# Optimization experiments

Hardware: AMD Instinct MI355X
Metric: run time of the kernel (lower is better)

## Reference

```python
import jax, jax.numpy as jnp
import numpy as np

B, T, D_MODEL = 2, 1024, 512
EXPAND = 2
D_INNER = D_MODEL * EXPAND
STATE = 16
K_CONV = 4


def setup_inputs() -> dict:
    key = jax.random.key(0)
    ks = jax.random.split(key, 10)
    sc = lambda k, shape: jax.random.normal(k, shape, jnp.float32) * 0.02
    return {
        "x": jax.random.normal(ks[0], (B, T, D_MODEL), jnp.float32),
        "ln_g": jnp.ones((D_MODEL,), jnp.float32),
        "ln_b": jnp.zeros((D_MODEL,), jnp.float32),
        "W_in": sc(ks[1], (2 * D_INNER, D_MODEL)),
        "conv_w": sc(ks[2], (D_INNER, 1, K_CONV)),
        "conv_b": jnp.zeros((D_INNER,), jnp.float32),
        "W_B": sc(ks[3], (STATE, D_INNER)),
        "W_C": sc(ks[4], (STATE, D_INNER)),
        "W_dt": sc(ks[5], (D_INNER, D_INNER)),
        "b_dt": jax.random.uniform(ks[6], (D_INNER,), jnp.float32, -4.0, -1.0),
        # log_A init: A_diag = -(n+1) from HiPPO, log(-A_diag) = log(n+1), broadcast over d_inner
        "log_A": jnp.broadcast_to(jnp.log(jnp.arange(1, STATE + 1, dtype=jnp.float32)), (D_INNER, STATE)),
        "W_out": sc(ks[7], (D_MODEL, D_INNER)),
    }


def _silu(v):
    return v * jax.nn.sigmoid(v)


def reference(x, ln_g, ln_b, W_in, conv_w, conv_b, W_B, W_C, W_dt, b_dt, log_A, W_out):
    residual = x
    # LayerNorm (biased variance, eps=1e-5)
    mu = x.mean(-1, keepdims=True)
    var = x.var(-1, keepdims=True)
    xn = (x - mu) * jax.lax.rsqrt(var + 1e-5) * ln_g + ln_b
    # input projection and gate split
    xz = xn @ W_in.T                      # (B,T,2*D_INNER)
    x_main, z = jnp.split(xz, 2, axis=-1)
    # depthwise causal conv1d (padding=3 then slice to T == left-pad 3)
    xc = jnp.transpose(x_main, (0, 2, 1))  # (B,D_INNER,T)
    xc = jax.lax.conv_general_dilated(
        xc, conv_w, window_strides=(1,), padding=[(K_CONV - 1, 0)],
        dimension_numbers=("NCH", "OIH", "NCH"), feature_group_count=D_INNER,
    ) + conv_b[None, :, None]
    x_main = _silu(jnp.transpose(xc, (0, 2, 1)))  # (B,T,D_INNER)
    # selective scan in fp32
    xf = x_main.astype(jnp.float32)
    Bt = xf @ W_B.T                        # (B,T,N)
    Ct = xf @ W_C.T                        # (B,T,N)
    dt = jax.nn.softplus(xf @ W_dt.T + b_dt)  # (B,T,D_INNER)
    A = -jnp.exp(log_A)                    # (D_INNER,N)
    dA = jnp.exp(A[None, None] * dt[..., None])              # (B,T,D_INNER,N)
    dBx = dt[..., None] * Bt[:, :, None, :] * xf[..., None]  # (B,T,D_INNER,N)

    def comb(c1, c2):
        a1, b1 = c1
        a2, b2 = c2
        return a1 * a2, a2 * b1 + b2

    _, h = jax.lax.associative_scan(comb, (dA, dBx), axis=1)  # h_t = dA_t*h_{t-1}+dBx_t
    y = (h * Ct[:, :, None, :]).sum(-1).astype(x.dtype)       # (B,T,D_INNER)
    out = (y * _silu(z)) @ W_out.T
    return residual + out
```

## Files before the change

### kernel.cpp

```cpp
#include <hip/hip_runtime.h>

#define T_SEQ 1024
#define DM 512
#define DI 1024
#define NS 16
#define NC 32
#define CL 32

typedef __attribute__((ext_vector_type(8))) short short8;
typedef __attribute__((ext_vector_type(4))) float f32x4;
typedef unsigned short u16;
typedef unsigned int u32;

__device__ inline float b2f(u16 u) {
    unsigned v = ((unsigned)u) << 16;
    return __builtin_bit_cast(float, v);
}
__device__ inline u16 f2b(float f) {
    unsigned u = __builtin_bit_cast(unsigned, f);
    u += 0x7fff + ((u >> 16) & 1);
    return (u16)(u >> 16);
}

__device__ inline void g2l16(const u16* g, const short* l) {
    __builtin_amdgcn_global_load_lds((const __attribute__((address_space(1))) u32*)g,
                                     (__attribute__((address_space(3))) u32*)l, 16, 0, 0);
}

template<int K> __device__ __forceinline__ void vmwait() {
    if constexpr (K == 0) asm volatile("s_waitcnt vmcnt(0)" ::: "memory");
    else if constexpr (K == 2) asm volatile("s_waitcnt vmcnt(2)" ::: "memory");
}

__global__ __launch_bounds__(256) void prep_k(const float* __restrict__ Win, const float* __restrict__ Wdt,
                       const float* __restrict__ Wout, const float* __restrict__ Wb,
                       const float* __restrict__ Wc,
                       u16* __restrict__ oWin, u16* __restrict__ wCat, u16* __restrict__ oWout,
                       const float* __restrict__ x, const float* __restrict__ g,
                       const float* __restrict__ be, u16* __restrict__ xn) {
    if (blockIdx.x < 2624) {
        int i = blockIdx.x * 256 + threadIdx.x;
        const float* s; u16* d; int off;
        if (i < 262144)      { s = Win;  d = oWin;  off = i; }
        else if (i < 524288) { s = Wdt;  d = wCat;  off = i - 262144; }
        else if (i < 655360) { s = Wout; d = oWout; off = i - 524288; }
        else if (i < 659456) { s = Wb;   d = wCat + 1048576; off = i - 655360; }
        else if (i < 663552) { s = Wc;   d = wCat + 1064960; off = i - 659456; }
        else {
            u16* dz = wCat + 1081344 + (i - 663552) * 4;
            dz[0] = 0; dz[1] = 0; dz[2] = 0; dz[3] = 0;
            return;
        }
        float4 v = ((const float4*)s)[off];
        d[off * 4 + 0] = f2b(v.x);
        d[off * 4 + 1] = f2b(v.y);
        d[off * 4 + 2] = f2b(v.z);
        d[off * 4 + 3] = f2b(v.w);
        return;
    }
    int row = blockIdx.x - 2624, tid = threadIdx.x;
    float2 v = ((const float2*)(x + row * DM))[tid];
    float s = v.x + v.y, q = v.x * v.x + v.y * v.y;
    #pragma unroll
    for (int m = 1; m < 64; m <<= 1) { s += __shfl_xor(s, m); q += __shfl_xor(q, m); }
    __shared__ float ss[4], qq[4];
    if ((tid & 63) == 0) { ss[tid >> 6] = s; qq[tid >> 6] = q; }
    __syncthreads();
    s = ss[0] + ss[1] + ss[2] + ss[3];
    q = qq[0] + qq[1] + qq[2] + qq[3];
    float mu = s / DM;
    float var = q / DM - mu * mu;
    float rs = rsqrtf(var + 1e-5f);
    int c = tid * 2;
    xn[row * DM + c]     = f2b((v.x - mu) * rs * g[c] + be[c]);
    xn[row * DM + c + 1] = f2b((v.y - mu) * rs * g[c + 1] + be[c + 1]);
}

template<int NT, int EPI>
__device__ __forceinline__ void gemm_core64(int bx, int by,
        const u16* __restrict__ A, int lda, const u16* __restrict__ Bw, int ldb,
        void* __restrict__ outp, int ldo, const float* __restrict__ extra,
        float* __restrict__ BtF, float* __restrict__ CtF) {
    __shared__ short a_sh[3 * 4096];
    __shared__ short b_sh[3 * 4096];
    int tid = threadIdx.x, w = tid >> 6, lane = tid & 63;
    int m0 = bx * 64, n0 = by * 64;
    int wr = (w >> 2) * 32, wc = (w & 3) * 16;
    int lr = lane & 15, kg = lane >> 4;
    f32x4 acc[2] = {};
    const u16* Abase = A + (size_t)m0 * lda;
    const u16* Bbase = Bw + (size_t)n0 * ldb;
    int lrow = lane >> 3;
    int cl = lane & 7;
    int row1 = w * 8 + lrow;
    int sc = cl ^ (row1 & 7);

    auto stage = [&](int buf, int kt) {
        int k0 = kt * 64;
        g2l16(Abase + (size_t)row1 * lda + k0 + sc * 8, a_sh + buf * 4096 + w * 512);
        g2l16(Bbase + (size_t)row1 * ldb + k0 + sc * 8, b_sh + buf * 4096 + w * 512);
    };

    stage(0, 0);
    stage(1, 1);
    for (int t = 0; t < NT; ++t) {
        if (t + 1 < NT) vmwait<2>();
        else vmwait<0>();
        __builtin_amdgcn_s_barrier();
        if (t + 2 < NT) stage((t + 2) % 3, t + 2);
        const short* as = a_sh + (t % 3) * 4096;
        const short* bs = b_sh + (t % 3) * 4096;
        int rsw = lr & 7;
        __builtin_amdgcn_s_setprio(1);
        #pragma unroll
        for (int kk = 0; kk < 2; ++kk) {
            short8 af[2], bfr;
            #pragma unroll
            for (int i = 0; i < 2; ++i) {
                int row = wr + i * 16 + lr;
                af[i] = *(const short8*)&as[row * 64 + ((kk * 4 + kg) ^ rsw) * 8];
            }
            {
                int row = wc + lr;
                bfr = *(const short8*)&bs[row * 64 + ((kk * 4 + kg) ^ rsw) * 8];
            }
            #pragma unroll
            for (int i = 0; i < 2; ++i)
                acc[i] = __builtin_amdgcn_mfma_f32_16x16x32_bf16(af[i], bfr, acc[i], 0, 0, 0);
        }
        __builtin_amdgcn_s_setprio(0);
    }

    int rb = (lane >> 4) * 4, cc = lane & 15;
    #pragma unroll
    for (int i = 0; i < 2; ++i) {
        #pragma unroll
        for (int r = 0; r < 4; ++r) {
            int row = m0 + wr + i * 16 + rb + r;
            int col = n0 + wc + cc;
            float v = acc[i][r];
            if (EPI == 0) {
                ((u16*)outp)[(size_t)row * ldo + col] = f2b(v);
            } else if (EPI == 2) {
                ((float*)outp)[(size_t)row * ldo + col] = v + extra[(size_t)row * ldo + col];
            } else if (EPI == 3) {
                ((float*)outp)[(size_t)row * ldo + col] = v;
            } else {
                if (col < 1024) {
                    float xx = v + extra[col];
                    float sp = (xx > 20.f) ? xx : log1pf(__expf(xx));
                    ((u16*)outp)[(size_t)row * ldo + col] = f2b(sp);
                } else if (col < 1040) {
                    BtF[(size_t)row * NS + (col - 1024)] = v;
                } else if (col < 1056) {
                    CtF[(size_t)row * NS + (col - 1040)] = v;
                }
            }
        }
    }
}

template<int NT, int EPI>
__global__ __launch_bounds__(512) void gemm8(int gx,
                                             const u16* __restrict__ A, int lda,
                                             const u16* __restrict__ Bw, int ldb,
                                             void* __restrict__ outp, int ldo,
                                             const float* __restrict__ extra,
                                             float* __restrict__ BtF, float* __restrict__ CtF) {
    int bx = blockIdx.x % gx, by = blockIdx.x / gx;
    gemm_core64<NT, EPI>(bx, by, A, lda, Bw, ldb, outp, ldo, extra, BtF, CtF);
}

__global__ __launch_bounds__(512) void gemm2_k(const u16* __restrict__ ym, const u16* __restrict__ Wout,
                                               float* __restrict__ p0, float* __restrict__ p1) {
    int bid = blockIdx.x;
    int ks = bid >> 8, rem = bid & 255;
    int bx = rem & 31, by = rem >> 5;
    float* p = ks ? p1 : p0;
    gemm_core64<8, 3>(bx, by, ym + ks * 512, DI, Wout + ks * 512, DI,
                      (void*)p, DM, nullptr, nullptr, nullptr);
}

__global__ __launch_bounds__(256) void merge_k(const float* __restrict__ p0, const float* __restrict__ p1,
                                               const float* __restrict__ x, float* __restrict__ out) {
    int i = blockIdx.x * 256 + threadIdx.x;
    float4 a = ((const float4*)p0)[i];
    float4 b = ((const float4*)p1)[i];
    float4 e = ((const float4*)x)[i];
    float4 o;
    o.x = a.x + b.x + e.x;
    o.y = a.y + b.y + e.y;
    o.z = a.z + b.z + e.z;
    o.w = a.w + b.w + e.w;
    ((float4*)out)[i] = o;
}

__global__ __launch_bounds__(256) void conv_k(const u16* __restrict__ xz, const float* __restrict__ w,
                                              const float* __restrict__ cb, u16* __restrict__ xf) {
    int base = (blockIdx.x * 256 + threadIdx.x) * 4;
    int d0 = base & (DI - 1);
    int bt = base >> 10;
    int t = bt & (T_SEQ - 1);
    float4 cbv = *(const float4*)(cb + d0);
    float s0 = cbv.x, s1 = cbv.y, s2 = cbv.z, s3 = cbv.w;
    float4 w0 = *(const float4*)(w + (d0 + 0) * 4);
    float4 w1 = *(const float4*)(w + (d0 + 1) * 4);
    float4 w2 = *(const float4*)(w + (d0 + 2) * 4);
    float4 w3 = *(const float4*)(w + (d0 + 3) * 4);
    const float* pw0 = (const float*)&w0;
    const float* pw1 = (const float*)&w1;
    const float* pw2 = (const float*)&w2;
    const float* pw3 = (const float*)&w3;
    #pragma unroll
    for (int i = 0; i < 4; ++i) {
        int tt = t - 3 + i;
        if (tt >= 0) {
            ushort4 xv = *(const ushort4*)(xz + (size_t)(bt - 3 + i) * 2048 + d0);
            s0 += pw0[i] * b2f(xv.x);
            s1 += pw1[i] * b2f(xv.y);
            s2 += pw2[i] * b2f(xv.z);
            s3 += pw3[i] * b2f(xv.w);
        }
    }
    ushort4 o;
    o.x = f2b(s0 / (1.f + __expf(-s0)));
    o.y = f2b(s1 / (1.f + __expf(-s1)));
    o.z = f2b(s2 / (1.f + __expf(-s2)));
    o.w = f2b(s3 / (1.f + __expf(-s3)));
    *(ushort4*)(xf + base) = o;
}

__global__ __launch_bounds__(256) void scanA(const u16* __restrict__ dt, const u16* __restrict__ xf,
                                             const float* __restrict__ Bt, const float* __restrict__ logA,
                                             float* __restrict__ Aprod, float* __restrict__ S) {
    int tid = threadIdx.x;
    int dblk = blockIdx.x & 3;
    int c = (blockIdx.x >> 2) & (NC - 1);
    int b = blockIdx.x >> 7;
    int d = dblk * 256 + tid;
    float Adn[NS], ap[NS], h[NS];
    #pragma unroll
    for (int j = 0; j < 4; ++j)
        *(float4*)&Adn[j * 4] = ((const float4*)(logA + (size_t)d * NS))[j];
    #pragma unroll
    for (int n = 0; n < NS; ++n) { Adn[n] = -__expf(Adn[n]); ap[n] = 1.f; h[n] = 0.f; }
    const u16* dtp = dt + ((size_t)b * T_SEQ + c * CL) * DI + d;
    const u16* xfp = xf + ((size_t)b * T_SEQ + c * CL) * DI + d;
    const float* Bp = Bt + ((size_t)b * T_SEQ + c * CL) * NS;
    #pragma unroll 8
    for (int i = 0; i < CL; ++i) {
        float dtv = b2f(dtp[(size_t)i * DI]);
        float xv  = b2f(xfp[(size_t)i * DI]);
        float ux = dtv * xv;
        float Bv[NS];
        #pragma unroll
        for (int j = 0; j < 4; ++j) *(float4*)&Bv[j * 4] = ((const float4*)(Bp + (size_t)i * NS))[j];
        #pragma unroll
        for (int n = 0; n < NS; ++n) {
            float dA = __expf(Adn[n] * dtv);
            h[n] = fmaf(dA, h[n], ux * Bv[n]);
            ap[n] *= dA;
        }
    }
    size_t o = ((((size_t)c * 2 + b) * DI) + d) * NS;
    #pragma unroll
    for (int j = 0; j < 4; ++j) {
        ((float4*)(Aprod + o))[j] = *(float4*)&ap[j * 4];
        ((float4*)(S + o))[j]     = *(float4*)&h[j * 4];
    }
}

__global__ __launch_bounds__(256) void scanB(const float* __restrict__ Aprod, const float* __restrict__ S,
                                             float* __restrict__ Hin) {
    int chain = blockIdx.x * 256 + threadIdx.x;
    float h = 0.f;
    #pragma unroll 8
    for (int c = 0; c < NC; ++c) {
        size_t o = (size_t)c * 32768 + chain;
        Hin[o] = h;
        h = fmaf(Aprod[o], h, S[o]);
    }
}

__global__ __launch_bounds__(256) void scanC(const u16* __restrict__ dt, const u16* __restrict__ xf,
                                             const float* __restrict__ Bt, const float* __restrict__ Ct,
                                             const float* __restrict__ logA, const float* __restrict__ Hin,
                                             const u16* __restrict__ xz, u16* __restrict__ ym) {
    int tid = threadIdx.x;
    int dblk = blockIdx.x & 3;
    int c = (blockIdx.x >> 2) & (NC - 1);
    int b = blockIdx.x >> 7;
    int d = dblk * 256 + tid;
    float Adn[NS], h[NS];
    #pragma unroll
    for (int j = 0; j < 4; ++j)
        *(float4*)&Adn[j * 4] = ((const float4*)(logA + (size_t)d * NS))[j];
    #pragma unroll
    for (int n = 0; n < NS; ++n) Adn[n] = -__expf(Adn[n]);
    size_t o = ((((size_t)c * 2 + b) * DI) + d) * NS;
    #pragma unroll
    for (int j = 0; j < 4; ++j) *(float4*)&h[j * 4] = ((const float4*)(Hin + o))[j];
    const u16* dtp = dt + ((size_t)b * T_SEQ + c * CL) * DI + d;
    const u16* xfp = xf + ((size_t)b * T_SEQ + c * CL) * DI + d;
    const float* Bp = Bt + ((size_t)b * T_SEQ + c * CL) * NS;
    const float* Cp = Ct + ((size_t)b * T_SEQ + c * CL) * NS;
    const u16* zp = xz + ((size_t)b * T_SEQ + c * CL) * 2048 + 1024 + d;
    u16* yp = ym + ((size_t)b * T_SEQ + c * CL) * DI + d;
    #pragma unroll 8
    for (int i = 0; i < CL; ++i) {
        float dtv = b2f(dtp[(size_t)i * DI]);
        float xv  = b2f(xfp[(size_t)i * DI]);
        float ux = dtv * xv;
        float Bv[NS], Cv[NS];
        #pragma unroll
        for (int j = 0; j < 4; ++j) {
            *(float4*)&Bv[j * 4] = ((const float4*)(Bp + (size_t)i * NS))[j];
            *(float4*)&Cv[j * 4] = ((const float4*)(Cp + (size_t)i * NS))[j];
        }
        float r = 0.f;
        #pragma unroll
        for (int n = 0; n < NS; ++n) {
            float dA = __expf(Adn[n] * dtv);
            h[n] = fmaf(dA, h[n], ux * Bv[n]);
            r = fmaf(h[n], Cv[n], r);
        }
        float zv = b2f(zp[(size_t)i * 2048]);
        float sz = zv / (1.f + __expf(-zv));
        yp[(size_t)i * DI] = f2b(r * sz);
    }
}

extern "C" void kernel_launch(void* const* d_in, const int* in_sizes, int n_in,
                              void* d_out, int out_size, void* d_ws, size_t ws_size,
                              hipStream_t stream) {
    const float* x     = (const float*)d_in[0];
    const float* ln_g  = (const float*)d_in[1];
    const float* ln_b  = (const float*)d_in[2];
    const float* W_in  = (const float*)d_in[3];
    const float* conv_w= (const float*)d_in[4];
    const float* conv_b= (const float*)d_in[5];
    const float* W_B   = (const float*)d_in[6];
    const float* W_C   = (const float*)d_in[7];
    const float* W_dt  = (const float*)d_in[8];
    const float* b_dt  = (const float*)d_in[9];
    const float* log_A = (const float*)d_in[10];
    const float* W_out = (const float*)d_in[11];

    char* ws = (char*)d_ws;
    u16* wInB  = (u16*)(ws + 0);
    u16* wCat  = (u16*)(ws + 2097152);
    u16* wOutB = (u16*)(ws + 4325376);
    u16* xnB   = (u16*)(ws + 5373952);
    u16* xzB   = (u16*)(ws + 7471104);
    u16* xfB   = (u16*)(ws + 15859712);
    u16* dtB   = (u16*)(ws + 20054016);
    float* BtF = (float*)(ws + 24248320);
    float* CtF = (float*)(ws + 24379392);
    u16* ymB   = (u16*)(ws + 24510464);
    float* ApF = (float*)(ws + 28704768);
    float* SF  = (float*)(ws + 32899072);
    float* HiF = (float*)(ws + 37093376);

    prep_k<<<4672, 256, 0, stream>>>(W_in, W_dt, W_out, W_B, W_C, wInB, wCat, wOutB,
                                     x, ln_g, ln_b, xnB);
    gemm8<8, 0><<<1024, 512, 0, stream>>>(32, xnB, 512, wInB, 512,
            (void*)xzB, 2048, nullptr, nullptr, nullptr);
    conv_k<<<2048, 256, 0, stream>>>(xzB, conv_w, conv_b, xfB);
    gemm8<16, 4><<<544, 512, 0, stream>>>(32, xfB, 1024, wCat, 1024,
            (void*)dtB, 1024, b_dt, BtF, CtF);
    scanA<<<256, 256, 0, stream>>>(dtB, xfB, BtF, log_A, ApF, SF);
    scanB<<<128, 256, 0, stream>>>(ApF, SF, HiF);
    scanC<<<256, 256, 0, stream>>>(dtB, xfB, BtF, CtF, log_A, HiF, xzB, ymB);
    gemm2_k<<<512, 512, 0, stream>>>(ymB, wOutB, ApF, SF);
    merge_k<<<1024, 256, 0, stream>>>(ApF, SF, x, (float*)d_out);
}
```

Baseline: 110.6 us.

## Use 128x64 block tiles with 4-wave 2x2 MFMA microtiles for input and dt GEMMs

Adds a new GEMM kernel using 128x64 output tiles per 256-thread block, with each wave computing a 64x32 tile (4x2 MFMA accumulators) over K-steps of 32 and a three-buffer global-to-LDS pipeline. It replaces the 64x64, 512-thread kernel for the input projection and the fused dt/B/C projection. The aim is more register-level reuse of A and B fragments and fewer LDS reads per MFMA. In exchange the grid is halved, which lowers parallelism, and the LDS layout drops the XOR swizzle, which may cause bank conflicts.

```diff
diff --git a/kernel.cpp b/kernel.cpp
--- a/kernel.cpp
+++ b/kernel.cpp
@@ -30,6 +30,7 @@
 template<int K> __device__ __forceinline__ void vmwait() {
     if constexpr (K == 0) asm volatile("s_waitcnt vmcnt(0)" ::: "memory");
     else if constexpr (K == 2) asm volatile("s_waitcnt vmcnt(2)" ::: "memory");
+    else if constexpr (K == 3) asm volatile("s_waitcnt vmcnt(3)" ::: "memory");
 }
 
 __global__ __launch_bounds__(256) void prep_k(const float* __restrict__ Win, const float* __restrict__ Wdt,
@@ -77,10 +78,87 @@
 }
 
 template<int NT, int EPI>
-__device__ __forceinline__ void gemm_core64(int bx, int by,
+__global__ __launch_bounds__(256) void gemm128(int gx,
         const u16* __restrict__ A, int lda, const u16* __restrict__ Bw, int ldb,
         void* __restrict__ outp, int ldo, const float* __restrict__ extra,
         float* __restrict__ BtF, float* __restrict__ CtF) {
+    __shared__ short a_sh[3 * 4096];
+    __shared__ short b_sh[3 * 2048];
+    int bx = blockIdx.x % gx, by = blockIdx.x / gx;
+    int tid = threadIdx.x, w = tid >> 6, lane = tid & 63;
+    int m0 = bx * 128, n0 = by * 64;
+    int wr = (w >> 1) * 64, wc = (w & 1) * 32;
+    int lr = lane & 15, kg = lane >> 4;
+    f32x4 acc[4][2] = {};
+    const u16* Abase = A + (size_t)m0 * lda;
+    const u16* Bbase = Bw + (size_t)n0 * ldb;
+    int srow = w * 16 + (lane >> 2);
+    int schunk = lane & 3;
+
+    auto stage = [&](int buf, int kt) {
+        int k0 = kt * 32;
+        g2l16(Abase + (size_t)srow * lda + k0 + schunk * 8, a_sh + buf * 4096 + w * 512);
+        g2l16(Abase + (size_t)(srow + 64) * lda + k0 + schunk * 8, a_sh + buf * 4096 + 2048 + w * 512);
+        g2l16(Bbase + (size_t)srow * ldb + k0 + schunk * 8, b_sh + buf * 2048 + w * 512);
+    };
+
+    stage(0, 0);
+    stage(1, 1);
+    for (int t = 0; t < NT; ++t) {
+        if (t + 1 < NT) vmwait<3>();
+        else vmwait<0>();
+        __builtin_amdgcn_s_barrier();
+        if (t + 2 < NT) stage((t + 2) % 3, t + 2);
+        const short* as = a_sh + (t % 3) * 4096;
+        const short* bs = b_sh + (t % 3) * 2048;
+        __builtin_amdgcn_s_setprio(1);
+        short8 af[4], bfr[2];
+        #pragma unroll
+        for (int i = 0; i < 4; ++i)
+            af[i] = *(const short8*)&as[(wr + i * 16 + lr) * 32 + kg * 8];
+        #pragma unroll
+        for (int j = 0; j < 2; ++j)
+            bfr[j] = *(const short8*)&bs[(wc + j * 16 + lr) * 32 + kg * 8];
+        #pragma unroll
+        for (int i = 0; i < 4; ++i)
+            #pragma unroll
+            for (int j = 0; j < 2; ++j)
+                acc[i][j] = __builtin_amdgcn_mfma_f32_16x16x32_bf16(af[i], bfr[j], acc[i][j], 0, 0, 0);
+        __builtin_amdgcn_s_setprio(0);
+    }
+
+    int rb = (lane >> 4) * 4, cc = lane & 15;
+    #pragma unroll
+    for (int i = 0; i < 4; ++i) {
+        #pragma unroll
+        for (int j = 0; j < 2; ++j) {
+            #pragma unroll
+            for (int r = 0; r < 4; ++r) {
+                int row = m0 + wr + i * 16 + rb + r;
+                int col = n0 + wc + j * 16 + cc;
+                float v = acc[i][j][r];
+                if (EPI == 0) {
+                    ((u16*)outp)[(size_t)row * ldo + col] = f2b(v);
+                } else {
+                    if (col < 1024) {
+                        float xx = v + extra[col];
+                        float sp = (xx > 20.f) ? xx : log1pf(__expf(xx));
+                        ((u16*)outp)[(size_t)row * ldo + col] = f2b(sp);
+                    } else if (col < 1040) {
+                        BtF[(size_t)row * NS + (col - 1024)] = v;
+                    } else if (col < 1056) {
+                        CtF[(size_t)row * NS + (col - 1040)] = v;
+                    }
+                }
+            }
+        }
+    }
+}
+
+template<int NT, int EPI>
+__device__ __forceinline__ void gemm_core64(int bx, int by,
+        const u16* __restrict__ A, int lda, const u16* __restrict__ Bw, int ldb,
+        void* __restrict__ outp, int ldo, const float* __restrict__ extra) {
     __shared__ short a_sh[3 * 4096];
     __shared__ short b_sh[3 * 4096];
     int tid = threadIdx.x, w = tid >> 6, lane = tid & 63;
@@ -139,36 +217,11 @@
             int row = m0 + wr + i * 16 + rb + r;
             int col = n0 + wc + cc;
             float v = acc[i][r];
-            if (EPI == 0) {
-                ((u16*)outp)[(size_t)row * ldo + col] = f2b(v);
-            } else if (EPI == 2) {
-                ((float*)outp)[(size_t)row * ldo + col] = v + extra[(size_t)row * ldo + col];
-            } else if (EPI == 3) {
+            if (EPI == 3) {
                 ((float*)outp)[(size_t)row * ldo + col] = v;
-            } else {
-                if (col < 1024) {
-                    float xx = v + extra[col];
-                    float sp = (xx > 20.f) ? xx : log1pf(__expf(xx));
-                    ((u16*)outp)[(size_t)row * ldo + col] = f2b(sp);
-                } else if (col < 1040) {
-                    BtF[(size_t)row * NS + (col - 1024)] = v;
-                } else if (col < 1056) {
-                    CtF[(size_t)row * NS + (col - 1040)] = v;
-                }
             }
         }
     }
-}
-
-template<int NT, int EPI>
-__global__ __launch_bounds__(512) void gemm8(int gx,
-                                             const u16* __restrict__ A, int lda,
-                                             const u16* __restrict__ Bw, int ldb,
-                                             void* __restrict__ outp, int ldo,
-                                             const float* __restrict__ extra,
-                                             float* __restrict__ BtF, float* __restrict__ CtF) {
-    int bx = blockIdx.x % gx, by = blockIdx.x / gx;
-    gemm_core64<NT, EPI>(bx, by, A, lda, Bw, ldb, outp, ldo, extra, BtF, CtF);
 }
 
 __global__ __launch_bounds__(512) void gemm2_k(const u16* __restrict__ ym, const u16* __restrict__ Wout,
@@ -178,7 +231,7 @@
     int bx = rem & 31, by = rem >> 5;
     float* p = ks ? p1 : p0;
     gemm_core64<8, 3>(bx, by, ym + ks * 512, DI, Wout + ks * 512, DI,
-                      (void*)p, DM, nullptr, nullptr, nullptr);
+                      (void*)p, DM, nullptr);
 }
 
 __global__ __launch_bounds__(256) void merge_k(const float* __restrict__ p0, const float* __restrict__ p1,
@@ -363,10 +416,10 @@
 
     prep_k<<<4672, 256, 0, stream>>>(W_in, W_dt, W_out, W_B, W_C, wInB, wCat, wOutB,
                                      x, ln_g, ln_b, xnB);
-    gemm8<8, 0><<<1024, 512, 0, stream>>>(32, xnB, 512, wInB, 512,
+    gemm128<16, 0><<<512, 256, 0, stream>>>(16, xnB, 512, wInB, 512,
             (void*)xzB, 2048, nullptr, nullptr, nullptr);
     conv_k<<<2048, 256, 0, stream>>>(xzB, conv_w, conv_b, xfB);
-    gemm8<16, 4><<<544, 512, 0, stream>>>(32, xfB, 1024, wCat, 1024,
+    gemm128<32, 4><<<272, 256, 0, stream>>>(16, xfB, 1024, wCat, 1024,
             (void*)dtB, 1024, b_dt, BtF, CtF);
     scanA<<<256, 256, 0, stream>>>(dtB, xfB, BtF, log_A, ApF, SF);
     scanB<<<128, 256, 0, stream>>>(ApF, SF, HiF);
```

Measured after the change: 124.7 us. +12.7%, slower.
